# Performance work log

Hardware: AMD Instinct MI355X
Metric: run time of the kernel (lower is better)

## Reference

```python
import jax, jax.numpy as jnp
import numpy as np

N_NODES = 100000
SIG_DIM = 64
N_ADJ = 1600000
N_QUERY = 262144


def setup_inputs() -> dict:
    key = jax.random.key(0)
    k1, k2, k3, k4, k5 = jax.random.split(key, 5)
    x = jax.random.normal(k1, (N_NODES, SIG_DIM), dtype=jnp.float32)
    x = x / jnp.linalg.norm(x, axis=1, keepdims=True)  # F.normalize(p=2, dim=1)
    node_weight = jax.random.uniform(k2, (N_NODES,), dtype=jnp.float32)
    edges = jax.random.randint(k3, (2, N_QUERY), 0, N_NODES)
    adj_row = jnp.sort(jax.random.randint(k4, (N_ADJ,), 0, N_NODES))
    adj_col = jax.random.randint(k5, (N_ADJ,), 0, N_NODES)
    return {
        "x": x,
        "node_weight": node_weight,
        "edges": edges,
        "adj_row": adj_row,
        "adj_col": adj_col,
        "num_nodes": N_NODES,
    }


def reference(x, node_weight, edges, adj_row, adj_col, num_nodes):
    # node signatures scaled by node weight
    xw = x * node_weight[:, None]                      # [N, D]

    seg = lambda vals: jax.ops.segment_sum(vals, adj_row, num_segments=num_nodes)

    # SpMM propagation: (A @ x)[i] = sum_{j in N(i)} x[j]
    one_hop = seg(xw[adj_col])                          # [N, D]
    deg = seg(jnp.ones_like(adj_row, dtype=xw.dtype))   # [N]
    two_iter = seg(one_hop[adj_col])                    # [N, D]

    # combine mode
    two_hop = two_iter - one_hop - xw
    deg2 = jnp.maximum(seg(deg[adj_col]) - deg - 1.0, 0.0)

    row, col = edges[0], edges[1]
    x_u_1 = one_hop[row]
    x_v_1 = one_hop[col]
    x_u_2 = two_hop[row]
    x_v_2 = two_hop[col]

    dot = lambda a, b: (a * b).sum(axis=-1)

    deg_u = deg[row]
    deg_v = deg[col]
    deg_u_2 = deg2[row]
    deg_v_2 = deg2[col]

    count_1_1 = dot(x_u_1, x_v_1)
    count_1_2 = dot(x_u_1, x_v_2)
    count_2_1 = dot(x_u_2, x_v_1)
    count_2_2 = dot(x_u_2, x_v_2)
    count_1_inf = deg_u + deg_v - 2 * count_1_1 - count_1_2 - count_2_1
    count_2_inf = deg_u_2 + deg_v_2 - 2 * count_2_2 - count_1_2 - count_2_1

    x_u_iter = two_iter[row]
    x_v_iter = two_iter[col]
    x_u = xw[row]
    x_v = xw[col]
    comb_count_1_2 = dot(x_u_1, x_v_iter)
    comb_count_2_1 = dot(x_u_iter, x_v_1)
    comb_count_2_2 = dot(x_u_iter - deg_u[:, None] * x_u,
                         x_v_iter - deg_v[:, None] * x_v)
    comb_count_self_1_2 = dot(x_u_1, x_u_iter)
    comb_count_self_2_1 = dot(x_v_1, x_v_iter)

    features = jnp.stack([
        count_1_1, count_1_2, count_2_1, count_2_2,
        count_1_inf, count_2_inf,
        comb_count_1_2, comb_count_2_1, comb_count_2_2,
        comb_count_self_1_2, comb_count_self_2_1,
        deg_u, deg_v, deg_u_2, deg_v_2,
    ], axis=1)                                          # [E, 15]
    return features
```

## Files before the change

kernel.cpp:

```cpp
#include <hip/hip_runtime.h>


#define D 64

typedef unsigned int uint32;
typedef _Float16 h2 __attribute__((ext_vector_type(2)));

union U32H2 { uint32 u; h2 h; };
__device__ __forceinline__ h2 u_as_h2(uint32 u) { U32H2 t; t.u = u; return t.h; }

__device__ __forceinline__ uint32 pack2(float a, float b) {
    uint32 ua = __float_as_uint(a);
    ua += 0x7fffu + ((ua >> 16) & 1u);
    uint32 ub = __float_as_uint(b);
    ub += 0x7fffu + ((ub >> 16) & 1u);
    return (ua >> 16) | (ub & 0xffff0000u);
}
__device__ __forceinline__ float lo2f(uint32 u) { return __uint_as_float(u << 16); }
__device__ __forceinline__ float hi2f(uint32 u) { return __uint_as_float(u & 0xffff0000u); }

__device__ __forceinline__ uint32 enc1(float v) {
    float a = fabsf(v);
    uint32 s = (__float_as_uint(v) >> 24) & 0x80u;
    if (a >= 448.f) return s | 0x7Eu;
    if (a < 0.015625f) {
        uint32 m = (uint32)rintf(a * 512.f);
        return (m > 7u) ? (s | 0x08u) : (s | m);
    }
    uint32 b = __float_as_uint(a);
    b += 0x7FFFFu + ((b >> 20) & 1u);
    uint32 m3 = (b >> 20) & 7u;
    int e4 = (int)(b >> 23) - 127 + 7;
    if (e4 > 15) return s | 0x7Eu;
    return s | ((uint32)e4 << 3) | m3;
}

__device__ __forceinline__ void dec8(uint32 u, uint32& pe, uint32& po) {
    uint32 se = (u << 8) & 0x80008000u;
    uint32 ue = u & 0x007f007fu;
    pe = ((ue << 7) + 0x08000800u) | se;
    uint32 so = u & 0x80008000u;
    uint32 uo = (u >> 8) & 0x007f007fu;
    po = ((uo << 7) + 0x08000800u) | so;
}

#define RED_GRP(v)  { v += __shfl_xor(v, 1, 64); v += __shfl_xor(v, 2, 64);  v += __shfl_xor(v, 4, 64);  }

__global__ void __launch_bounds__(256) prep_kernel(const float4* __restrict__ x,
                                                   const float* __restrict__ w,
                                                   uint2* __restrict__ xw,
                                                   const int* __restrict__ adj_row,
                                                   int* __restrict__ row_ptr,
                                                   int n8, int n, int nadj, int xw_blocks) {
    if ((int)blockIdx.x < xw_blocks) {
        int i = blockIdx.x * blockDim.x + threadIdx.x;
        if (i >= n8) return;
        float s = w[i >> 3] * 64.f;
        float4 a = x[i * 2], b = x[i * 2 + 1];
        uint32 w0 = enc1(a.x * s) | (enc1(a.z * s) << 8)
                  | (enc1(a.y * s) << 16) | (enc1(a.w * s) << 24);
        uint32 w1 = enc1(b.x * s) | (enc1(b.z * s) << 8)
                  | (enc1(b.y * s) << 16) | (enc1(b.w * s) << 24);
        xw[i] = make_uint2(w0, w1);
    } else {
        int i = (blockIdx.x - xw_blocks) * blockDim.x + threadIdx.x;
        if (i > n) return;
        int lo = 0, hi = nadj;
        while (lo < hi) {
            int mid = (lo + hi) >> 1;
            if (adj_row[mid] < i) lo = mid + 1; else hi = mid;
        }
        row_ptr[i] = lo;
    }
}

__global__ void __launch_bounds__(256) spmm1_kernel(const uint2* __restrict__ src,
                                                    const int* __restrict__ row_ptr,
                                                    const int* __restrict__ adj_col,
                                                    uint4* __restrict__ dst,
                                                    float* __restrict__ degout,
                                                    int n) {
    int lane = threadIdx.x & 63;
    int sub = lane & 7;
    int node = blockIdx.x * 32 + (threadIdx.x >> 6) * 8 + (lane >> 3);
    if (node >= n) return;
    int start = row_ptr[node], end = row_ptr[node + 1];
    int deg_n = end - start;
    h2 acc0 = u_as_h2(0u), acc1 = u_as_h2(0u), acc2 = u_as_h2(0u), acc3 = u_as_h2(0u);
    int gbase = lane & 56;
    const int* colp = adj_col + start;
    int base = 0;
    for (; base + 8 <= deg_n; base += 8) {
        int idx = colp[base + sub];
#pragma unroll
        for (int i = 0; i < 8; ++i) {
            int c = __shfl(idx, gbase + i, 64);
            uint2 qv = src[(size_t)c * 8 + sub];
            uint32 pe, po;
            dec8(qv.x, pe, po);
            acc0 += u_as_h2(pe); acc1 += u_as_h2(po);
            dec8(qv.y, pe, po);
            acc2 += u_as_h2(pe); acc3 += u_as_h2(po);
        }
    }
    if (base < deg_n) {
        int k = base + sub;
        int idx = (k < deg_n) ? colp[k] : 0;
#pragma unroll
        for (int i = 0; i < 8; ++i) {
            if (base + i < deg_n) {
                int c = __shfl(idx, gbase + i, 64);
                uint2 qv = src[(size_t)c * 8 + sub];
                uint32 pe, po;
                dec8(qv.x, pe, po);
                acc0 += u_as_h2(pe); acc1 += u_as_h2(po);
                dec8(qv.y, pe, po);
                acc2 += u_as_h2(pe); acc3 += u_as_h2(po);
            }
        }
    }
    uint4 o;
    o.x = pack2((float)acc0.x, (float)acc0.y);
    o.y = pack2((float)acc1.x, (float)acc1.y);
    o.z = pack2((float)acc2.x, (float)acc2.y);
    o.w = pack2((float)acc3.x, (float)acc3.y);
    dst[(size_t)node * 8 + sub] = o;
    if (sub == 0) degout[node] = (float)deg_n;
}

__global__ void __launch_bounds__(256) spmm2_kernel(const uint4* __restrict__ src,
                                                    const int* __restrict__ row_ptr,
                                                    const int* __restrict__ adj_col,
                                                    const float* __restrict__ degv,
                                                    uint4* __restrict__ dst,
                                                    float2* __restrict__ degpair,
                                                    int n) {
    int lane = threadIdx.x & 63;
    int sub = lane & 7;
    int node = blockIdx.x * 32 + (threadIdx.x >> 6) * 8 + (lane >> 3);
    if (node >= n) return;
    int start = row_ptr[node], end = row_ptr[node + 1];
    int deg_n = end - start;
    float a0 = 0.f, a1 = 0.f, a2 = 0.f, a3 = 0.f,
          a4 = 0.f, a5 = 0.f, a6 = 0.f, a7 = 0.f;
    float dsum = 0.f;
    int gbase = lane & 56;
    const int* colp = adj_col + start;
    int base = 0;
    for (; base + 8 <= deg_n; base += 8) {
        int idx = colp[base + sub];
        dsum += degv[idx];
#pragma unroll
        for (int i = 0; i < 8; ++i) {
            int c = __shfl(idx, gbase + i, 64);
            uint4 qv = src[(size_t)c * 8 + sub];
            a0 += lo2f(qv.x); a1 += hi2f(qv.x);
            a2 += lo2f(qv.y); a3 += hi2f(qv.y);
            a4 += lo2f(qv.z); a5 += hi2f(qv.z);
            a6 += lo2f(qv.w); a7 += hi2f(qv.w);
        }
    }
    if (base < deg_n) {
        int k = base + sub;
        bool kv = k < deg_n;
        int idx = kv ? colp[k] : 0;
        if (kv) dsum += degv[idx];
#pragma unroll
        for (int i = 0; i < 8; ++i) {
            if (base + i < deg_n) {
                int c = __shfl(idx, gbase + i, 64);
                uint4 qv = src[(size_t)c * 8 + sub];
                a0 += lo2f(qv.x); a1 += hi2f(qv.x);
                a2 += lo2f(qv.y); a3 += hi2f(qv.y);
                a4 += lo2f(qv.z); a5 += hi2f(qv.z);
                a6 += lo2f(qv.w); a7 += hi2f(qv.w);
            }
        }
    }
    uint4 o;
    o.x = pack2(a0, a1); o.y = pack2(a2, a3);
    o.z = pack2(a4, a5); o.w = pack2(a6, a7);
    dst[(size_t)node * 8 + sub] = o;
    RED_GRP(dsum)
    if (sub == 0)
        degpair[node] = make_float2((float)deg_n,
                                    fmaxf(dsum - (float)deg_n - 1.0f, 0.0f));
}

__global__ void __launch_bounds__(256) edge_kernel(const int* __restrict__ edges,
                                                   const uint2* __restrict__ xw,
                                                   const uint4* __restrict__ h1,
                                                   const uint4* __restrict__ t2,
                                                   const float2* __restrict__ degpair,
                                                   float* __restrict__ out,
                                                   int E) {
    int t = blockIdx.x * blockDim.x + threadIdx.x;
    int q = t >> 3, sub = t & 7;
    if (q >= E) return;
    int u = edges[q], v = edges[E + q];
    uint2 pxu = xw[(size_t)u * 8 + sub], pxv = xw[(size_t)v * 8 + sub];
    uint4 phu = h1[(size_t)u * 8 + sub], phv = h1[(size_t)v * 8 + sub];
    uint4 ptu = t2[(size_t)u * 8 + sub], ptv = t2[(size_t)v * 8 + sub];
    float2 dpu = degpair[u], dpv = degpair[v];
    float du = dpu.x, du2 = dpu.y, dv = dpv.x, dv2 = dpv.y;

    float fxu[8], fxv[8], fhu[8], fhv[8], ftu[8], ftv[8];
    {
        uint32 pe, po;
        dec8(pxu.x, pe, po);
        h2 e = u_as_h2(pe), o_ = u_as_h2(po);
        fxu[0] = (float)e.x; fxu[1] = (float)e.y; fxu[2] = (float)o_.x; fxu[3] = (float)o_.y;
        dec8(pxu.y, pe, po);
        e = u_as_h2(pe); o_ = u_as_h2(po);
        fxu[4] = (float)e.x; fxu[5] = (float)e.y; fxu[6] = (float)o_.x; fxu[7] = (float)o_.y;
        dec8(pxv.x, pe, po);
        e = u_as_h2(pe); o_ = u_as_h2(po);
        fxv[0] = (float)e.x; fxv[1] = (float)e.y; fxv[2] = (float)o_.x; fxv[3] = (float)o_.y;
        dec8(pxv.y, pe, po);
        e = u_as_h2(pe); o_ = u_as_h2(po);
        fxv[4] = (float)e.x; fxv[5] = (float)e.y; fxv[6] = (float)o_.x; fxv[7] = (float)o_.y;
    }
    fhu[0]=lo2f(phu.x); fhu[1]=hi2f(phu.x); fhu[2]=lo2f(phu.y); fhu[3]=hi2f(phu.y);
    fhu[4]=lo2f(phu.z); fhu[5]=hi2f(phu.z); fhu[6]=lo2f(phu.w); fhu[7]=hi2f(phu.w);
    fhv[0]=lo2f(phv.x); fhv[1]=hi2f(phv.x); fhv[2]=lo2f(phv.y); fhv[3]=hi2f(phv.y);
    fhv[4]=lo2f(phv.z); fhv[5]=hi2f(phv.z); fhv[6]=lo2f(phv.w); fhv[7]=hi2f(phv.w);
    ftu[0]=lo2f(ptu.x); ftu[1]=hi2f(ptu.x); ftu[2]=lo2f(ptu.y); ftu[3]=hi2f(ptu.y);
    ftu[4]=lo2f(ptu.z); ftu[5]=hi2f(ptu.z); ftu[6]=lo2f(ptu.w); ftu[7]=hi2f(ptu.w);
    ftv[0]=lo2f(ptv.x); ftv[1]=hi2f(ptv.x); ftv[2]=lo2f(ptv.y); ftv[3]=hi2f(ptv.y);
    ftv[4]=lo2f(ptv.z); ftv[5]=hi2f(ptv.z); ftv[6]=lo2f(ptv.w); ftv[7]=hi2f(ptv.w);

    float c11 = 0.f, c12 = 0.f, c21 = 0.f, c22 = 0.f,
          cc12 = 0.f, cc21 = 0.f, cc22 = 0.f, cs12 = 0.f, cs21 = 0.f;
#pragma unroll
    for (int j = 0; j < 8; ++j) {
        float xu = fxu[j], xv = fxv[j];
        float hu = fhu[j], hv = fhv[j];
        float tu = ftu[j], tv = ftv[j];
        float h2u = tu - hu - xu, h2v = tv - hv - xv;
        float au = fmaf(-du, xu, tu), av = fmaf(-dv, xv, tv);
        c11  = fmaf(hu,  hv,  c11);
        c12  = fmaf(hu,  h2v, c12);
        c21  = fmaf(h2u, hv,  c21);
        c22  = fmaf(h2u, h2v, c22);
        cc12 = fmaf(hu,  tv,  cc12);
        cc21 = fmaf(tu,  hv,  cc21);
        cc22 = fmaf(au,  av,  cc22);
        cs12 = fmaf(hu,  tu,  cs12);
        cs21 = fmaf(hv,  tv,  cs21);
    }
    RED_GRP(c11) RED_GRP(c12) RED_GRP(c21) RED_GRP(c22)
    RED_GRP(cc12) RED_GRP(cc21) RED_GRP(cc22) RED_GRP(cs12) RED_GRP(cs21)

    if (sub == 0) {
        float* o = out + (size_t)q * 15;
        o[0]  = c11;
        o[1]  = c12;
        o[2]  = c21;
        o[3]  = c22;
        o[4]  = du + dv - 2.f * c11 - c12 - c21;
        o[5]  = du2 + dv2 - 2.f * c22 - c12 - c21;
        o[6]  = cc12;
        o[7]  = cc21;
        o[8]  = cc22;
        o[9]  = cs12;
        o[10] = cs21;
        o[11] = du;
        o[12] = dv;
        o[13] = du2;
        o[14] = dv2;
    }
}

extern "C" void kernel_launch(void* const* d_in, const int* in_sizes, int n_in,
                              void* d_out, int out_size, void* d_ws, size_t ws_size,
                              hipStream_t stream) {
    const float* x       = (const float*)d_in[0];
    const float* w       = (const float*)d_in[1];
    const int*   edges   = (const int*)d_in[2];
    const int*   adj_row = (const int*)d_in[3];
    const int*   adj_col = (const int*)d_in[4];

    const int N    = in_sizes[1];
    const int E    = in_sizes[2] / 2;
    const int NADJ = in_sizes[3];

    char* ws = (char*)d_ws;
    size_t off = 0;
    auto take = [&](size_t bytes) {
        void* p = ws + off;
        off = (off + bytes + 255) & ~(size_t)255;
        return p;
    };
    uint2*  xw      = (uint2*)take((size_t)N * 8 * sizeof(uint2));
    uint4*  one_hop = (uint4*)take((size_t)N * D * 2);
    uint4*  two_it  = (uint4*)take((size_t)N * D * 2);
    float*  deg     = (float*)take((size_t)N * sizeof(float));
    float2* degpair = (float2*)take((size_t)N * sizeof(float2));
    int*    row_ptr = (int*)take((size_t)(N + 1) * sizeof(int));
    (void)ws_size;

    float* out = (float*)d_out;

    {
        int n8 = N * 8;
        int xw_blocks = (n8 + 255) / 256;
        int rp_blocks = (N + 1 + 255) / 256;
        prep_kernel<<<xw_blocks + rp_blocks, 256, 0, stream>>>(
            (const float4*)x, w, xw, adj_row, row_ptr, n8, N, NADJ, xw_blocks);
    }
    spmm1_kernel<<<(N + 31) / 32, 256, 0, stream>>>(xw, row_ptr, adj_col, one_hop, deg, N);
    spmm2_kernel<<<(N + 31) / 32, 256, 0, stream>>>(one_hop, row_ptr, adj_col, deg,
                                                    two_it, degpair, N);
    edge_kernel<<<((size_t)E * 8 + 255) / 256, 256, 0, stream>>>(edges, xw, one_hop, two_it,
                                                                 degpair, out, E);
}
```

Measured before the change: 185.8 us.

## Store one-hop in fp8 and stage edge outputs through shared memory

The one-hop intermediate is now encoded as 8-bit floats (scaled by 64) instead of bf16, which halves the bytes gathered in spmm2 and the edge kernel. spmm2 accumulates in packed fp16 instead of fp32. The edge kernel also writes its 15 features per edge into shared memory first and then stores them to global memory contiguously, so writes coalesce. The cost is lower precision on one-hop and possible fp16 overflow or accuracy loss in the two-hop accumulation.

```diff
diff --git a/kernel.cpp b/kernel.cpp
--- a/kernel.cpp
+++ b/kernel.cpp
@@ -42,6 +42,18 @@
     uint32 so = u & 0x80008000u;
     uint32 uo = (u >> 8) & 0x007f007fu;
     po = ((uo << 7) + 0x08000800u) | so;
+}
+
+__device__ __forceinline__ uint2 enc8(h2 a0, h2 a1, h2 a2, h2 a3) {
+    uint32 w0 = enc1((float)a0.x * 64.f)
+              | (enc1((float)a1.x * 64.f) << 8)
+              | (enc1((float)a0.y * 64.f) << 16)
+              | (enc1((float)a1.y * 64.f) << 24);
+    uint32 w1 = enc1((float)a2.x * 64.f)
+              | (enc1((float)a3.x * 64.f) << 8)
+              | (enc1((float)a2.y * 64.f) << 16)
+              | (enc1((float)a3.y * 64.f) << 24);
+    return make_uint2(w0, w1);
 }
 
 #define RED_GRP(v)  { v += __shfl_xor(v, 1, 64); v += __shfl_xor(v, 2, 64);  v += __shfl_xor(v, 4, 64);  }
@@ -77,7 +89,7 @@
 __global__ void __launch_bounds__(256) spmm1_kernel(const uint2* __restrict__ src,
                                                     const int* __restrict__ row_ptr,
                                                     const int* __restrict__ adj_col,
-                                                    uint4* __restrict__ dst,
+                                                    uint2* __restrict__ dst,
                                                     float* __restrict__ degout,
                                                     int n) {
     int lane = threadIdx.x & 63;
@@ -119,16 +131,11 @@
             }
         }
     }
-    uint4 o;
-    o.x = pack2((float)acc0.x, (float)acc0.y);
-    o.y = pack2((float)acc1.x, (float)acc1.y);
-    o.z = pack2((float)acc2.x, (float)acc2.y);
-    o.w = pack2((float)acc3.x, (float)acc3.y);
-    dst[(size_t)node * 8 + sub] = o;
+    dst[(size_t)node * 8 + sub] = enc8(acc0, acc1, acc2, acc3);
     if (sub == 0) degout[node] = (float)deg_n;
 }
 
-__global__ void __launch_bounds__(256) spmm2_kernel(const uint4* __restrict__ src,
+__global__ void __launch_bounds__(256) spmm2_kernel(const uint2* __restrict__ src,
                                                     const int* __restrict__ row_ptr,
                                                     const int* __restrict__ adj_col,
                                                     const float* __restrict__ degv,
@@ -141,8 +148,7 @@
     if (node >= n) return;
     int start = row_ptr[node], end = row_ptr[node + 1];
     int deg_n = end - start;
-    float a0 = 0.f, a1 = 0.f, a2 = 0.f, a3 = 0.f,
-          a4 = 0.f, a5 = 0.f, a6 = 0.f, a7 = 0.f;
+    h2 acc0 = u_as_h2(0u), acc1 = u_as_h2(0u), acc2 = u_as_h2(0u), acc3 = u_as_h2(0u);
     float dsum = 0.f;
     int gbase = lane & 56;
     const int* colp = adj_col + start;
@@ -153,11 +159,12 @@
 #pragma unroll
         for (int i = 0; i < 8; ++i) {
             int c = __shfl(idx, gbase + i, 64);
-            uint4 qv = src[(size_t)c * 8 + sub];
-            a0 += lo2f(qv.x); a1 += hi2f(qv.x);
-            a2 += lo2f(qv.y); a3 += hi2f(qv.y);
-            a4 += lo2f(qv.z); a5 += hi2f(qv.z);
-            a6 += lo2f(qv.w); a7 += hi2f(qv.w);
+            uint2 qv = src[(size_t)c * 8 + sub];
+            uint32 pe, po;
+            dec8(qv.x, pe, po);
+            acc0 += u_as_h2(pe); acc1 += u_as_h2(po);
+            dec8(qv.y, pe, po);
+            acc2 += u_as_h2(pe); acc3 += u_as_h2(po);
         }
     }
     if (base < deg_n) {
@@ -169,17 +176,20 @@
         for (int i = 0; i < 8; ++i) {
             if (base + i < deg_n) {
                 int c = __shfl(idx, gbase + i, 64);
-                uint4 qv = src[(size_t)c * 8 + sub];
-                a0 += lo2f(qv.x); a1 += hi2f(qv.x);
-                a2 += lo2f(qv.y); a3 += hi2f(qv.y);
-                a4 += lo2f(qv.z); a5 += hi2f(qv.z);
-                a6 += lo2f(qv.w); a7 += hi2f(qv.w);
+                uint2 qv = src[(size_t)c * 8 + sub];
+                uint32 pe, po;
+                dec8(qv.x, pe, po);
+                acc0 += u_as_h2(pe); acc1 += u_as_h2(po);
+                dec8(qv.y, pe, po);
+                acc2 += u_as_h2(pe); acc3 += u_as_h2(po);
             }
         }
     }
     uint4 o;
-    o.x = pack2(a0, a1); o.y = pack2(a2, a3);
-    o.z = pack2(a4, a5); o.w = pack2(a6, a7);
+    o.x = pack2((float)acc0.x, (float)acc0.y);
+    o.y = pack2((float)acc1.x, (float)acc1.y);
+    o.z = pack2((float)acc2.x, (float)acc2.y);
+    o.w = pack2((float)acc3.x, (float)acc3.y);
     dst[(size_t)node * 8 + sub] = o;
     RED_GRP(dsum)
     if (sub == 0)
@@ -189,85 +199,96 @@
 
 __global__ void __launch_bounds__(256) edge_kernel(const int* __restrict__ edges,
                                                    const uint2* __restrict__ xw,
-                                                   const uint4* __restrict__ h1,
+                                                   const uint2* __restrict__ h1,
                                                    const uint4* __restrict__ t2,
                                                    const float2* __restrict__ degpair,
                                                    float* __restrict__ out,
                                                    int E) {
+    __shared__ float so[32 * 15];
     int t = blockIdx.x * blockDim.x + threadIdx.x;
     int q = t >> 3, sub = t & 7;
-    if (q >= E) return;
-    int u = edges[q], v = edges[E + q];
-    uint2 pxu = xw[(size_t)u * 8 + sub], pxv = xw[(size_t)v * 8 + sub];
-    uint4 phu = h1[(size_t)u * 8 + sub], phv = h1[(size_t)v * 8 + sub];
-    uint4 ptu = t2[(size_t)u * 8 + sub], ptv = t2[(size_t)v * 8 + sub];
-    float2 dpu = degpair[u], dpv = degpair[v];
-    float du = dpu.x, du2 = dpu.y, dv = dpv.x, dv2 = dpv.y;
-
-    float fxu[8], fxv[8], fhu[8], fhv[8], ftu[8], ftv[8];
-    {
-        uint32 pe, po;
-        dec8(pxu.x, pe, po);
-        h2 e = u_as_h2(pe), o_ = u_as_h2(po);
-        fxu[0] = (float)e.x; fxu[1] = (float)e.y; fxu[2] = (float)o_.x; fxu[3] = (float)o_.y;
-        dec8(pxu.y, pe, po);
-        e = u_as_h2(pe); o_ = u_as_h2(po);
-        fxu[4] = (float)e.x; fxu[5] = (float)e.y; fxu[6] = (float)o_.x; fxu[7] = (float)o_.y;
-        dec8(pxv.x, pe, po);
-        e = u_as_h2(pe); o_ = u_as_h2(po);
-        fxv[0] = (float)e.x; fxv[1] = (float)e.y; fxv[2] = (float)o_.x; fxv[3] = (float)o_.y;
-        dec8(pxv.y, pe, po);
-        e = u_as_h2(pe); o_ = u_as_h2(po);
-        fxv[4] = (float)e.x; fxv[5] = (float)e.y; fxv[6] = (float)o_.x; fxv[7] = (float)o_.y;
-    }
-    fhu[0]=lo2f(phu.x); fhu[1]=hi2f(phu.x); fhu[2]=lo2f(phu.y); fhu[3]=hi2f(phu.y);
-    fhu[4]=lo2f(phu.z); fhu[5]=hi2f(phu.z); fhu[6]=lo2f(phu.w); fhu[7]=hi2f(phu.w);
-    fhv[0]=lo2f(phv.x); fhv[1]=hi2f(phv.x); fhv[2]=lo2f(phv.y); fhv[3]=hi2f(phv.y);
-    fhv[4]=lo2f(phv.z); fhv[5]=hi2f(phv.z); fhv[6]=lo2f(phv.w); fhv[7]=hi2f(phv.w);
-    ftu[0]=lo2f(ptu.x); ftu[1]=hi2f(ptu.x); ftu[2]=lo2f(ptu.y); ftu[3]=hi2f(ptu.y);
-    ftu[4]=lo2f(ptu.z); ftu[5]=hi2f(ptu.z); ftu[6]=lo2f(ptu.w); ftu[7]=hi2f(ptu.w);
-    ftv[0]=lo2f(ptv.x); ftv[1]=hi2f(ptv.x); ftv[2]=lo2f(ptv.y); ftv[3]=hi2f(ptv.y);
-    ftv[4]=lo2f(ptv.z); ftv[5]=hi2f(ptv.z); ftv[6]=lo2f(ptv.w); ftv[7]=hi2f(ptv.w);
-
-    float c11 = 0.f, c12 = 0.f, c21 = 0.f, c22 = 0.f,
-          cc12 = 0.f, cc21 = 0.f, cc22 = 0.f, cs12 = 0.f, cs21 = 0.f;
-#pragma unroll
-    for (int j = 0; j < 8; ++j) {
-        float xu = fxu[j], xv = fxv[j];
-        float hu = fhu[j], hv = fhv[j];
-        float tu = ftu[j], tv = ftv[j];
-        float h2u = tu - hu - xu, h2v = tv - hv - xv;
-        float au = fmaf(-du, xu, tu), av = fmaf(-dv, xv, tv);
-        c11  = fmaf(hu,  hv,  c11);
-        c12  = fmaf(hu,  h2v, c12);
-        c21  = fmaf(h2u, hv,  c21);
-        c22  = fmaf(h2u, h2v, c22);
-        cc12 = fmaf(hu,  tv,  cc12);
-        cc21 = fmaf(tu,  hv,  cc21);
-        cc22 = fmaf(au,  av,  cc22);
-        cs12 = fmaf(hu,  tu,  cs12);
-        cs21 = fmaf(hv,  tv,  cs21);
-    }
-    RED_GRP(c11) RED_GRP(c12) RED_GRP(c21) RED_GRP(c22)
-    RED_GRP(cc12) RED_GRP(cc21) RED_GRP(cc22) RED_GRP(cs12) RED_GRP(cs21)
-
-    if (sub == 0) {
-        float* o = out + (size_t)q * 15;
-        o[0]  = c11;
-        o[1]  = c12;
-        o[2]  = c21;
-        o[3]  = c22;
-        o[4]  = du + dv - 2.f * c11 - c12 - c21;
-        o[5]  = du2 + dv2 - 2.f * c22 - c12 - c21;
-        o[6]  = cc12;
-        o[7]  = cc21;
-        o[8]  = cc22;
-        o[9]  = cs12;
-        o[10] = cs21;
-        o[11] = du;
-        o[12] = dv;
-        o[13] = du2;
-        o[14] = dv2;
+    bool valid = q < E;
+    if (valid) {
+        int u = edges[q], v = edges[E + q];
+        uint2 pxu = xw[(size_t)u * 8 + sub], pxv = xw[(size_t)v * 8 + sub];
+        uint2 phu = h1[(size_t)u * 8 + sub], phv = h1[(size_t)v * 8 + sub];
+        uint4 ptu = t2[(size_t)u * 8 + sub], ptv = t2[(size_t)v * 8 + sub];
+        float2 dpu = degpair[u], dpv = degpair[v];
+        float du = dpu.x, du2 = dpu.y, dv = dpv.x, dv2 = dpv.y;
+
+        float fxu[8], fxv[8], fhu[8], fhv[8], ftu[8], ftv[8];
+        {
+            uint32 pe, po;
+            h2 e, o_;
+#define DEC_F8(P, F)                                                     \
+            dec8(P.x, pe, po);                                           \
+            e = u_as_h2(pe); o_ = u_as_h2(po);                           \
+            F[0] = (float)e.x; F[1] = (float)e.y;                        \
+            F[2] = (float)o_.x; F[3] = (float)o_.y;                      \
+            dec8(P.y, pe, po);                                           \
+            e = u_as_h2(pe); o_ = u_as_h2(po);                           \
+            F[4] = (float)e.x; F[5] = (float)e.y;                        \
+            F[6] = (float)o_.x; F[7] = (float)o_.y;
+            DEC_F8(pxu, fxu)
+            DEC_F8(pxv, fxv)
+            DEC_F8(phu, fhu)
+            DEC_F8(phv, fhv)
+#undef DEC_F8
+        }
+        ftu[0]=lo2f(ptu.x); ftu[1]=hi2f(ptu.x); ftu[2]=lo2f(ptu.y); ftu[3]=hi2f(ptu.y);
+        ftu[4]=lo2f(ptu.z); ftu[5]=hi2f(ptu.z); ftu[6]=lo2f(ptu.w); ftu[7]=hi2f(ptu.w);
+        ftv[0]=lo2f(ptv.x); ftv[1]=hi2f(ptv.x); ftv[2]=lo2f(ptv.y); ftv[3]=hi2f(ptv.y);
+        ftv[4]=lo2f(ptv.z); ftv[5]=hi2f(ptv.z); ftv[6]=lo2f(ptv.w); ftv[7]=hi2f(ptv.w);
+
+        float c11 = 0.f, c12 = 0.f, c21 = 0.f, c22 = 0.f,
+              cc12 = 0.f, cc21 = 0.f, cc22 = 0.f, cs12 = 0.f, cs21 = 0.f;
+#pragma unroll
+        for (int j = 0; j < 8; ++j) {
+            float xu = fxu[j], xv = fxv[j];
+            float hu = fhu[j], hv = fhv[j];
+            float tu = ftu[j], tv = ftv[j];
+            float h2u = tu - hu - xu, h2v = tv - hv - xv;
+            float au = fmaf(-du, xu, tu), av = fmaf(-dv, xv, tv);
+            c11  = fmaf(hu,  hv,  c11);
+            c12  = fmaf(hu,  h2v, c12);
+            c21  = fmaf(h2u, hv,  c21);
+            c22  = fmaf(h2u, h2v, c22);
+            cc12 = fmaf(hu,  tv,  cc12);
+            cc21 = fmaf(tu,  hv,  cc21);
+            cc22 = fmaf(au,  av,  cc22);
+            cs12 = fmaf(hu,  tu,  cs12);
+            cs21 = fmaf(hv,  tv,  cs21);
+        }
+        RED_GRP(c11) RED_GRP(c12) RED_GRP(c21) RED_GRP(c22)
+        RED_GRP(cc12) RED_GRP(cc21) RED_GRP(cc22) RED_GRP(cs12) RED_GRP(cs21)
+
+        if (sub == 0) {
+            float* o = so + (threadIdx.x >> 3) * 15;
+            o[0]  = c11;
+            o[1]  = c12;
+            o[2]  = c21;
+            o[3]  = c22;
+            o[4]  = du + dv - 2.f * c11 - c12 - c21;
+            o[5]  = du2 + dv2 - 2.f * c22 - c12 - c21;
+            o[6]  = cc12;
+            o[7]  = cc21;
+            o[8]  = cc22;
+            o[9]  = cs12;
+            o[10] = cs21;
+            o[11] = du;
+            o[12] = dv;
+            o[13] = du2;
+            o[14] = dv2;
+        }
+    }
+    __syncthreads();
+    int eb = blockIdx.x * 32;
+    if (eb < E) {
+        int nval = E - eb; if (nval > 32) nval = 32;
+        int nflt = nval * 15;
+        size_t obase = (size_t)eb * 15;
+        for (int k = threadIdx.x; k < nflt; k += 256)
+            out[obase + k] = so[k];
     }
 }
 
@@ -292,7 +313,7 @@
         return p;
     };
     uint2*  xw      = (uint2*)take((size_t)N * 8 * sizeof(uint2));
-    uint4*  one_hop = (uint4*)take((size_t)N * D * 2);
+    uint2*  one_hop = (uint2*)take((size_t)N * 8 * sizeof(uint2));
     uint4*  two_it  = (uint4*)take((size_t)N * D * 2);
     float*  deg     = (float*)take((size_t)N * sizeof(float));
     float2* degpair = (float2*)take((size_t)N * sizeof(float2));
```

After: 184.6 us. No clear change (-0.7%).
